# Kernel tuning notes

Measured on AMD Instinct MI355X. Metric: run time of the kernel, lower is better.

## Reference

```python
import jax, jax.numpy as jnp
import numpy as np

NUM_HEADS = 8
NUM_GROUPS = 32
EMB = 512
EPS = 1e-5


def setup_inputs() -> dict:
    key = jax.random.key(0)
    ks = jax.random.split(key, 12)
    B, C, H, W = 256, EMB, 16, 16
    s = 1.0 / np.sqrt(C)
    x = jax.random.normal(ks[0], (B, C, H, W), dtype=jnp.float32)
    Wq = jax.random.normal(ks[1], (C, EMB), dtype=jnp.float32) * s
    bq = jax.random.normal(ks[2], (EMB,), dtype=jnp.float32) * 0.01
    Wk = jax.random.normal(ks[3], (C, EMB), dtype=jnp.float32) * s
    bk = jax.random.normal(ks[4], (EMB,), dtype=jnp.float32) * 0.01
    Wv = jax.random.normal(ks[5], (C, EMB), dtype=jnp.float32) * s
    bv = jax.random.normal(ks[6], (EMB,), dtype=jnp.float32) * 0.01
    Wf = jax.random.normal(ks[7], (EMB, EMB), dtype=jnp.float32) * s
    bf = jax.random.normal(ks[8], (EMB,), dtype=jnp.float32) * 0.01
    gn_w = jnp.ones((EMB,), dtype=jnp.float32)
    gn_b = jnp.zeros((EMB,), dtype=jnp.float32)
    return {"x": x, "Wq": Wq, "bq": bq, "Wk": Wk, "bk": bk,
            "Wv": Wv, "bv": bv, "Wf": Wf, "bf": bf,
            "gn_w": gn_w, "gn_b": gn_b}


def reference(x, Wq, bq, Wk, bk, Wv, bv, Wf, bf, gn_w, gn_b):
    B, C, H, W = x.shape
    S = H * W
    nh = NUM_HEADS
    dh = EMB // nh
    xs = x.reshape(B, C, S).transpose(0, 2, 1)  # [B, S, C]
    q = (xs @ Wq + bq).reshape(B, S, nh, dh)
    k = (xs @ Wk + bk).reshape(B, S, nh, dh)
    v = (xs @ Wv + bv).reshape(B, S, nh, dh)
    scale = dh ** -0.5
    logits = jnp.einsum('bshd,bthd->bhst', q, k) * scale  # [B, nh, S, S]
    attn = jax.nn.softmax(logits, axis=-1)
    o = jnp.einsum('bhst,bthd->bshd', attn, v).reshape(B, S, EMB)
    o = o @ Wf + bf  # [B, S, EMB]
    y = o.transpose(0, 2, 1).reshape(B, EMB, H, W) + x  # residual
    # GroupNorm over (channels-within-group, H, W)
    G = NUM_GROUPS
    yg = y.reshape(B, G, EMB // G, H, W)
    mu = jnp.mean(yg, axis=(2, 3, 4), keepdims=True)
    var = jnp.var(yg, axis=(2, 3, 4), keepdims=True)
    yn = ((yg - mu) * jax.lax.rsqrt(var + EPS)).reshape(B, EMB, H, W)
    return yn * gn_w.reshape(1, EMB, 1, 1) + gn_b.reshape(1, EMB, 1, 1)
```

## Files before the change

### kernel.cpp

```cpp
#include <hip/hip_runtime.h>
#include <hip/hip_bf16.h>
#include <stdint.h>

#define B_  256
#define C_  512
#define S_  256
#define NH  8
#define DH  64

typedef float f32x4 __attribute__((ext_vector_type(4)));
typedef short s16x8 __attribute__((ext_vector_type(8)));

static __device__ __forceinline__ unsigned short f2bf(float f) {
  union { float f; unsigned u; } v; v.f = f;
  unsigned r = v.u + 0x7FFFu + ((v.u >> 16) & 1u);
  return (unsigned short)(r >> 16);
}

static __device__ __forceinline__ unsigned pk_bf16(float lo, float hi) {
  unsigned r;
  asm("v_cvt_pk_bf16_f32 %0, %1, %2" : "=v"(r) : "v"(lo), "v"(hi));
  return r;
}

static __device__ __forceinline__ void gload_lds16(const void* g, void* l) {
  __builtin_amdgcn_global_load_lds((const __attribute__((address_space(1))) void*)g,
                                   (__attribute__((address_space(3))) void*)l,
                                   16, 0, 0);
}

__global__ __launch_bounds__(256) void prep(const float* __restrict__ x,
                                            const float* __restrict__ Wq,
                                            const float* __restrict__ Wk,
                                            const float* __restrict__ Wv,
                                            const float* __restrict__ Wf,
                                            unsigned short* __restrict__ Whead,
                                            unsigned short* __restrict__ Wft,
                                            unsigned short* __restrict__ xs) {
  __shared__ float tile[64][65];
  int bid = blockIdx.x;
  int t = threadIdx.x;
  int tr = t >> 4;
  int tc = (t & 15) * 4;
  if (bid < 8192) {
    int b = bid >> 5, rem = bid & 31;
    int s0 = (rem & 3) * 64, c0 = (rem >> 2) * 64;
    const float* xb = x + (size_t)b * C_ * S_;
#pragma unroll
    for (int i = 0; i < 4; ++i) {
      int c = tr + i * 16;
      float4 v = *(const float4*)&xb[(size_t)(c0 + c) * S_ + s0 + tc];
      tile[c][tc + 0] = v.x; tile[c][tc + 1] = v.y;
      tile[c][tc + 2] = v.z; tile[c][tc + 3] = v.w;
    }
    __syncthreads();
    unsigned short* xsb = xs + (size_t)b * S_ * C_;
#pragma unroll
    for (int i = 0; i < 4; ++i) {
      int s = tr + i * 16;
      ushort4 o;
      o.x = f2bf(tile[tc + 0][s]); o.y = f2bf(tile[tc + 1][s]);
      o.z = f2bf(tile[tc + 2][s]); o.w = f2bf(tile[tc + 3][s]);
      *(ushort4*)&xsb[(size_t)(s0 + s) * C_ + c0 + tc] = o;
    }
  } else {
    int r = bid - 8192;
    int mat = r >> 6, r6 = r & 63;
    int n0 = (r6 & 7) * 64, c0 = (r6 >> 3) * 64;
    const float* src = (mat == 0) ? Wq : (mat == 1) ? Wk : (mat == 2) ? Wv : Wf;
#pragma unroll
    for (int i = 0; i < 4; ++i) {
      int c = tr + i * 16;
      float4 v = *(const float4*)&src[(size_t)(c0 + c) * 512 + n0 + tc];
      tile[c][tc + 0] = v.x; tile[c][tc + 1] = v.y;
      tile[c][tc + 2] = v.z; tile[c][tc + 3] = v.w;
    }
    __syncthreads();
    int h = n0 >> 6;
    unsigned short* dst = (mat < 3) ? (Whead + ((size_t)h * 192 + mat * 64) * 512)
                                    : (Wft + (size_t)n0 * 512);
#pragma unroll
    for (int i = 0; i < 4; ++i) {
      int nl = tr + i * 16;
      ushort4 o;
      o.x = f2bf(tile[tc + 0][nl]); o.y = f2bf(tile[tc + 1][nl]);
      o.z = f2bf(tile[tc + 2][nl]); o.w = f2bf(tile[tc + 3][nl]);
      *(ushort4*)&dst[(size_t)nl * 512 + c0 + tc] = o;
    }
  }
}

#define QKP 68
#define QOFF 0
#define KOFF 34816
#define VOFF 69632
__global__ __launch_bounds__(512) void qkvattn(const unsigned short* __restrict__ xs,
                                               const unsigned short* __restrict__ Whead,
                                               const float* __restrict__ bq,
                                               const float* __restrict__ bk,
                                               const float* __restrict__ bv,
                                               unsigned short* __restrict__ o) {
  __shared__ __align__(16) char lds[114688];
  int bid = blockIdx.x;
  int lin = (bid & 7) * 256 + (bid >> 3);
  int h = lin & 7, b = lin >> 3;
  int t = threadIdx.x, lane = t & 63, w = t >> 6;
  int l15 = lane & 15, l4 = lane >> 4;
  int wr = w >> 2, wc = w & 3;
  const unsigned short* xsb = xs + (size_t)b * S_ * C_;
  const unsigned short* wh  = Whead + (size_t)h * 192 * C_;

#define FSTAGE(kt, p)                                                         \
  {                                                                           \
    _Pragma("unroll")                                                         \
    for (int i = 0; i < 4; ++i) {                                             \
      int ch = i * 512 + t, r = ch >> 3, g = ch & 7;                          \
      int gs = g ^ (r & 7);                                                   \
      gload_lds16(xsb + (size_t)r * C_ + (kt) * 64 + gs * 8,                  \
                  lds + (p) * 57344 + ch * 16);                               \
    }                                                                         \
    _Pragma("unroll")                                                         \
    for (int i = 0; i < 3; ++i) {                                             \
      int ch = i * 512 + t, r = ch >> 3, g = ch & 7;                          \
      int gs = g ^ (r & 7);                                                   \
      gload_lds16(wh + (size_t)r * C_ + (kt) * 64 + gs * 8,                   \
                  lds + (p) * 57344 + 32768 + ch * 16);                       \
    }                                                                         \
  }

  f32x4 acc[8][3] = {};
  FSTAGE(0, 0);

  for (int kt = 0; kt < 8; ++kt) {
    if (kt < 7) FSTAGE(kt + 1, (kt + 1) & 1);
    if (kt < 7) asm volatile("s_waitcnt vmcnt(7)" ::: "memory");
    else        asm volatile("s_waitcnt vmcnt(0)" ::: "memory");
    __builtin_amdgcn_s_barrier();
    asm volatile("" ::: "memory");
    const char* Ab = lds + (kt & 1) * 57344;
    const char* Bb = Ab + 32768;
#pragma unroll
    for (int kk = 0; kk < 2; ++kk) {
      s16x8 afr[8], bfr[3];
#pragma unroll
      for (int fi = 0; fi < 8; ++fi) {
        int r = wr * 128 + fi * 16 + l15;
        afr[fi] = *(const s16x8*)(Ab + r * 128 + (((kk * 4 + l4) ^ (r & 7)) << 4));
      }
#pragma unroll
      for (int fj = 0; fj < 3; ++fj) {
        int r = wc * 48 + fj * 16 + l15;
        bfr[fj] = *(const s16x8*)(Bb + r * 128 + (((kk * 4 + l4) ^ (r & 7)) << 4));
      }
      __builtin_amdgcn_s_setprio(1);
#pragma unroll
      for (int fi = 0; fi < 8; ++fi)
#pragma unroll
        for (int fj = 0; fj < 3; ++fj)
          acc[fi][fj] = __builtin_amdgcn_mfma_f32_16x16x32_bf16(afr[fi], bfr[fj], acc[fi][fj], 0, 0, 0);
      __builtin_amdgcn_s_setprio(0);
    }
    __builtin_amdgcn_s_barrier();
  }
#undef FSTAGE

  unsigned short* Ql = (unsigned short*)(lds + QOFF);
  unsigned short* Kl = (unsigned short*)(lds + KOFF);
  unsigned short* Vl = (unsigned short*)(lds + VOFF);
  int h64 = h * 64;
#pragma unroll
  for (int fj = 0; fj < 3; ++fj) {
    int n = wc * 48 + fj * 16 + l15;
    int sel = n >> 6, d = n & 63;
    const float* bias = (sel == 0) ? bq : (sel == 1) ? bk : bv;
    float bias_v = bias[h64 + d];
    if (sel == 2) {
#pragma unroll
      for (int fi = 0; fi < 8; ++fi) {
        int s0 = wr * 128 + fi * 16 + l4 * 4;
        ushort4 o4;
        o4.x = f2bf(acc[fi][fj][0] + bias_v);
        o4.y = f2bf(acc[fi][fj][1] + bias_v);
        o4.z = f2bf(acc[fi][fj][2] + bias_v);
        o4.w = f2bf(acc[fi][fj][3] + bias_v);
        *(ushort4*)&Vl[d * 264 + s0] = o4;
      }
    } else {
      unsigned short* dstl = (sel == 0) ? Ql : Kl;
#pragma unroll
      for (int fi = 0; fi < 8; ++fi)
#pragma unroll
        for (int rg = 0; rg < 4; ++rg) {
          int s = wr * 128 + fi * 16 + l4 * 4 + rg;
          int row = s;
          if (sel == 1) {
            int s64 = s & 63, w32 = s64 & 31;
            row = (s & 192) + (s64 >> 5) * 32 + ((w32 >> 2) & 1) * 16 + (w32 >> 3) * 4 + (w32 & 3);
          }
          dstl[row * QKP + d] = f2bf(acc[fi][fj][rg] + bias_v);
        }
    }
  }
  __syncthreads();

  s16x8 qf[2][2];
#pragma unroll
  for (int fi = 0; fi < 2; ++fi)
#pragma unroll
    for (int kk = 0; kk < 2; ++kk) {
      int row = w * 32 + fi * 16 + l15;
      qf[fi][kk] = *(const s16x8*)((const char*)lds + QOFF + row * (QKP * 2) + kk * 64 + l4 * 16);
    }

  f32x4 acco[4][2] = {};
  float m_run[2] = {-3e38f, -3e38f}, l_run[2] = {0.f, 0.f};
  const float SCL = 0.125f * 1.44269504089f;

  for (int kb = 0; kb < 4; ++kb) {
    f32x4 accs[4][2] = {};
#pragma unroll
    for (int kk = 0; kk < 2; ++kk) {
      s16x8 kf[4];
#pragma unroll
      for (int fj = 0; fj < 4; ++fj)
        kf[fj] = *(const s16x8*)((const char*)lds + KOFF + (kb * 64 + fj * 16 + l15) * (QKP * 2) + kk * 64 + l4 * 16);
      __builtin_amdgcn_s_setprio(1);
#pragma unroll
      for (int fj = 0; fj < 4; ++fj)
#pragma unroll
        for (int fi = 0; fi < 2; ++fi)
          accs[fj][fi] = __builtin_amdgcn_mfma_f32_16x16x32_bf16(kf[fj], qf[fi][kk], accs[fj][fi], 0, 0, 0);
      __builtin_amdgcn_s_setprio(0);
    }
#pragma unroll
    for (int fi = 0; fi < 2; ++fi) {
      float m0[4];
#pragma unroll
      for (int fj = 0; fj < 4; ++fj)
        m0[fj] = fmaxf(fmaxf(accs[fj][fi][0], accs[fj][fi][1]),
                       fmaxf(accs[fj][fi][2], accs[fj][fi][3]));
      float mx = fmaxf(fmaxf(m0[0], m0[1]), fmaxf(m0[2], m0[3]));
      mx = fmaxf(mx, __shfl_xor(mx, 16, 64));
      mx = fmaxf(mx, __shfl_xor(mx, 32, 64));
      float mnew = fmaxf(m_run[fi], mx);
      float alpha = __builtin_amdgcn_exp2f((m_run[fi] - mnew) * SCL);
      m_run[fi] = mnew;
      float s0[4];
#pragma unroll
      for (int fj = 0; fj < 4; ++fj) {
#pragma unroll
        for (int rg = 0; rg < 4; ++rg) {
          float p = __builtin_amdgcn_exp2f((accs[fj][fi][rg] - mnew) * SCL);
          accs[fj][fi][rg] = p;
        }
        s0[fj] = (accs[fj][fi][0] + accs[fj][fi][1]) + (accs[fj][fi][2] + accs[fj][fi][3]);
      }
      float lsum = (s0[0] + s0[1]) + (s0[2] + s0[3]);
      lsum += __shfl_xor(lsum, 16, 64);
      lsum += __shfl_xor(lsum, 32, 64);
      l_run[fi] = l_run[fi] * alpha + lsum;
#pragma unroll
      for (int fd = 0; fd < 4; ++fd)
#pragma unroll
        for (int rg = 0; rg < 4; ++rg) acco[fd][fi][rg] *= alpha;
    }
#pragma unroll
    for (int kk2 = 0; kk2 < 2; ++kk2) {
      s16x8 vf[4];
#pragma unroll
      for (int fd = 0; fd < 4; ++fd)
        vf[fd] = *(const s16x8*)((const char*)lds + VOFF + (fd * 16 + l15) * 528 + kb * 128 + kk2 * 64 + l4 * 16);
#pragma unroll
      for (int fi = 0; fi < 2; ++fi) {
        union { unsigned u[4]; s16x8 v; } pb;
        pb.u[0] = pk_bf16(accs[2 * kk2][fi][0],     accs[2 * kk2][fi][1]);
        pb.u[1] = pk_bf16(accs[2 * kk2][fi][2],     accs[2 * kk2][fi][3]);
        pb.u[2] = pk_bf16(accs[2 * kk2 + 1][fi][0], accs[2 * kk2 + 1][fi][1]);
        pb.u[3] = pk_bf16(accs[2 * kk2 + 1][fi][2], accs[2 * kk2 + 1][fi][3]);
        __builtin_amdgcn_s_setprio(1);
#pragma unroll
        for (int fd = 0; fd < 4; ++fd)
          acco[fd][fi] = __builtin_amdgcn_mfma_f32_16x16x32_bf16(vf[fd], pb.v, acco[fd][fi], 0, 0, 0);
        __builtin_amdgcn_s_setprio(0);
      }
    }
  }

  unsigned short* ob = o + (size_t)b * S_ * C_ + h * DH;
#pragma unroll
  for (int fi = 0; fi < 2; ++fi) {
    float inv = 1.0f / l_run[fi];
    int qrow = w * 32 + fi * 16 + l15;
#pragma unroll
    for (int fd = 0; fd < 4; ++fd) {
      ushort4 s4;
      s4.x = f2bf(acco[fd][fi][0] * inv);
      s4.y = f2bf(acco[fd][fi][1] * inv);
      s4.z = f2bf(acco[fd][fi][2] * inv);
      s4.w = f2bf(acco[fd][fi][3] * inv);
      *(ushort4*)&ob[(size_t)qrow * C_ + fd * 16 + l4 * 4] = s4;
    }
  }
}

__global__ __launch_bounds__(512) void proj_gn(const unsigned short* __restrict__ o,
                                               const unsigned short* __restrict__ Wft,
                                               const float* __restrict__ bfp,
                                               const float* __restrict__ x,
                                               const float* __restrict__ gnw,
                                               const float* __restrict__ gnb,
                                               float* __restrict__ out) {
  __shared__ __align__(16) char plds[98304];
  __shared__ float red_s[128], red_q[128];
  __shared__ float mu_s[8], rs_s[8];
  int bid = blockIdx.x;
  int lin = (bid & 7) * 128 + (bid >> 3);
  int b = lin >> 2, ct = lin & 3;
  int t = threadIdx.x, lane = t & 63, w = t >> 6;
  int l15 = lane & 15, l4 = lane >> 4;
  int wc = w >> 2, wsq = w & 3;
  if (t < 128) { red_s[t] = 0.f; red_q[t] = 0.f; }
  f32x4 acc[4][4] = {};
  const unsigned short* wt = Wft + (size_t)ct * 128 * C_;
  const unsigned short* ob = o + (size_t)b * S_ * C_;

#define PSTAGE(kt, p)                                                         \
  {                                                                           \
    _Pragma("unroll")                                                         \
    for (int i = 0; i < 2; ++i) {                                             \
      int ch = i * 512 + t, r = ch >> 3, g = ch & 7;                          \
      int gs = g ^ (r & 7);                                                   \
      gload_lds16(wt + (size_t)r * C_ + (kt) * 64 + gs * 8,                   \
                  plds + (p) * 49152 + ch * 16);                              \
    }                                                                         \
    _Pragma("unroll")                                                         \
    for (int i = 0; i < 4; ++i) {                                             \
      int ch = i * 512 + t, r = ch >> 3, g = ch & 7;                          \
      int gs = g ^ (r & 7);                                                   \
      gload_lds16(ob + (size_t)r * C_ + (kt) * 64 + gs * 8,                   \
                  plds + (p) * 49152 + 16384 + ch * 16);                      \
    }                                                                         \
  }

  PSTAGE(0, 0);

  for (int kt = 0; kt < 8; ++kt) {
    if (kt < 7) PSTAGE(kt + 1, (kt + 1) & 1);
    if (kt < 7) asm volatile("s_waitcnt vmcnt(6)" ::: "memory");
    else        asm volatile("s_waitcnt vmcnt(0)" ::: "memory");
    __builtin_amdgcn_s_barrier();
    asm volatile("" ::: "memory");
    const char* Ab = plds + (kt & 1) * 49152;
    const char* Bb = Ab + 16384;
#pragma unroll
    for (int kk = 0; kk < 2; ++kk) {
      s16x8 af[4], bfr[4];
#pragma unroll
      for (int fi = 0; fi < 4; ++fi) {
        int r = wc * 64 + fi * 16 + l15;
        af[fi] = *(const s16x8*)(Ab + r * 128 + (((kk * 4 + l4) ^ (r & 7)) << 4));
      }
#pragma unroll
      for (int fj = 0; fj < 4; ++fj) {
        int r = wsq * 64 + fj * 16 + l15;
        bfr[fj] = *(const s16x8*)(Bb + r * 128 + (((kk * 4 + l4) ^ (r & 7)) << 4));
      }
      __builtin_amdgcn_s_setprio(1);
#pragma unroll
      for (int fi = 0; fi < 4; ++fi)
#pragma unroll
        for (int fj = 0; fj < 4; ++fj)
          acc[fi][fj] = __builtin_amdgcn_mfma_f32_16x16x32_bf16(af[fi], bfr[fj], acc[fi][fj], 0, 0, 0);
      __builtin_amdgcn_s_setprio(0);
    }
    __builtin_amdgcn_s_barrier();
  }
#undef PSTAGE

  const float* xb = x + (size_t)b * C_ * S_;
  int c_base = ct * 128 + wc * 64;
  int s_base = wsq * 64;
#pragma unroll
  for (int fi = 0; fi < 4; ++fi)
#pragma unroll
    for (int rg = 0; rg < 4; ++rg) {
      int c = c_base + fi * 16 + l4 * 4 + rg;
      float bias_v = bfp[c];
      float psum = 0.f, psq = 0.f;
#pragma unroll
      for (int fj = 0; fj < 4; ++fj) {
        int s = s_base + fj * 16 + l15;
        float y = acc[fi][fj][rg] + bias_v + xb[(size_t)c * S_ + s];
        acc[fi][fj][rg] = y;
        psum += y; psq += y * y;
      }
#pragma unroll
      for (int off = 1; off < 16; off <<= 1) {
        psum += __shfl_xor(psum, off, 64);
        psq += __shfl_xor(psq, off, 64);
      }
      if (l15 == 0) {
        int cl = c - ct * 128;
        atomicAdd(&red_s[cl], psum);
        atomicAdd(&red_q[cl], psq);
      }
    }
  __syncthreads();
  if (t < 8) {
    float s = 0.f, qq = 0.f;
#pragma unroll
    for (int i = 0; i < 16; ++i) { s += red_s[t * 16 + i]; qq += red_q[t * 16 + i]; }
    float mu = s * (1.0f / 4096.0f);
    float var = qq * (1.0f / 4096.0f) - mu * mu;
    mu_s[t] = mu;
    rs_s[t] = rsqrtf(var + 1e-5f);
  }
  __syncthreads();
  float* outb = out + (size_t)b * C_ * S_;
#pragma unroll
  for (int fi = 0; fi < 4; ++fi)
#pragma unroll
    for (int rg = 0; rg < 4; ++rg) {
      int c = c_base + fi * 16 + l4 * 4 + rg;
      int gl = (c - ct * 128) >> 4;
      float mu = mu_s[gl], rs = rs_s[gl];
      float gw = gnw[c], gb = gnb[c];
#pragma unroll
      for (int fj = 0; fj < 4; ++fj) {
        int s = s_base + fj * 16 + l15;
        outb[(size_t)c * S_ + s] = (acc[fi][fj][rg] - mu) * rs * gw + gb;
      }
    }
}

extern "C" void kernel_launch(void* const* d_in, const int* in_sizes, int n_in,
                              void* d_out, int out_size, void* d_ws, size_t ws_size,
                              hipStream_t stream) {
  const float* x   = (const float*)d_in[0];
  const float* Wq  = (const float*)d_in[1];
  const float* bq  = (const float*)d_in[2];
  const float* Wk  = (const float*)d_in[3];
  const float* bk  = (const float*)d_in[4];
  const float* Wv  = (const float*)d_in[5];
  const float* bv  = (const float*)d_in[6];
  const float* Wf  = (const float*)d_in[7];
  const float* bf  = (const float*)d_in[8];
  const float* gnw = (const float*)d_in[9];
  const float* gnb = (const float*)d_in[10];

  char* ws = (char*)d_ws;
  unsigned short* Whead = (unsigned short*)ws;
  unsigned short* Wft   = (unsigned short*)(ws + 0x180000);
  unsigned short* xs    = (unsigned short*)(ws + 0x200000);
  unsigned short* obuf  = (unsigned short*)(ws + 0x200000 + (size_t)B_ * S_ * C_ * 2);
  float* out = (float*)d_out;

  hipLaunchKernelGGL(prep, dim3(8448), dim3(256), 0, stream,
                     x, Wq, Wk, Wv, Wf, Whead, Wft, xs);
  hipLaunchKernelGGL(qkvattn, dim3(2048), dim3(512), 0, stream,
                     xs, Whead, bq, bk, bv, obuf);
  hipLaunchKernelGGL(proj_gn, dim3(1024), dim3(512), 0, stream,
                     obuf, Wft, bf, x, gnw, gnb, out);
}
```

Measured before the change: 315.3 us.

## Shrink proj_gn tiles to 64 channels and K-step 32 for higher occupancy

```diff
diff --git a/kernel.cpp b/kernel.cpp
--- a/kernel.cpp
+++ b/kernel.cpp
@@ -303,92 +303,92 @@
   }
 }
 
-__global__ __launch_bounds__(512) void proj_gn(const unsigned short* __restrict__ o,
-                                               const unsigned short* __restrict__ Wft,
-                                               const float* __restrict__ bfp,
-                                               const float* __restrict__ x,
-                                               const float* __restrict__ gnw,
-                                               const float* __restrict__ gnb,
-                                               float* __restrict__ out) {
-  __shared__ __align__(16) char plds[98304];
-  __shared__ float red_s[128], red_q[128];
-  __shared__ float mu_s[8], rs_s[8];
+__global__ __launch_bounds__(512, 4) void proj_gn(const unsigned short* __restrict__ o,
+                                                  const unsigned short* __restrict__ Wft,
+                                                  const float* __restrict__ bfp,
+                                                  const float* __restrict__ x,
+                                                  const float* __restrict__ gnw,
+                                                  const float* __restrict__ gnb,
+                                                  float* __restrict__ out) {
+  __shared__ __align__(16) char plds[40960];
+  __shared__ float red_s[64], red_q[64];
+  __shared__ float mu_s[4], rs_s[4];
   int bid = blockIdx.x;
-  int lin = (bid & 7) * 128 + (bid >> 3);
-  int b = lin >> 2, ct = lin & 3;
+  int lin = (bid & 7) * 256 + (bid >> 3);
+  int b = lin >> 3, ct = lin & 7;
   int t = threadIdx.x, lane = t & 63, w = t >> 6;
   int l15 = lane & 15, l4 = lane >> 4;
-  int wc = w >> 2, wsq = w & 3;
-  if (t < 128) { red_s[t] = 0.f; red_q[t] = 0.f; }
-  f32x4 acc[4][4] = {};
-  const unsigned short* wt = Wft + (size_t)ct * 128 * C_;
+  if (t < 64) { red_s[t] = 0.f; red_q[t] = 0.f; }
+  f32x4 acc[4][2] = {};
+  const unsigned short* wt = Wft + (size_t)ct * 64 * C_;
   const unsigned short* ob = o + (size_t)b * S_ * C_;
 
 #define PSTAGE(kt, p)                                                         \
   {                                                                           \
+    if (t < 256) {                                                            \
+      int r = t >> 2, g = t & 3;                                              \
+      int gs = g ^ ((r >> 1) & 3);                                            \
+      gload_lds16(wt + (size_t)r * C_ + (kt) * 32 + gs * 8,                   \
+                  plds + (p) * 20480 + t * 16);                               \
+    }                                                                         \
     _Pragma("unroll")                                                         \
     for (int i = 0; i < 2; ++i) {                                             \
-      int ch = i * 512 + t, r = ch >> 3, g = ch & 7;                          \
-      int gs = g ^ (r & 7);                                                   \
-      gload_lds16(wt + (size_t)r * C_ + (kt) * 64 + gs * 8,                   \
-                  plds + (p) * 49152 + ch * 16);                              \
+      int ch = i * 512 + t, r = ch >> 2, g = ch & 3;                          \
+      int gs = g ^ ((r >> 1) & 3);                                            \
+      gload_lds16(ob + (size_t)r * C_ + (kt) * 32 + gs * 8,                   \
+                  plds + (p) * 20480 + 4096 + ch * 16);                       \
     }                                                                         \
-    _Pragma("unroll")                                                         \
-    for (int i = 0; i < 4; ++i) {                                             \
-      int ch = i * 512 + t, r = ch >> 3, g = ch & 7;                          \
-      int gs = g ^ (r & 7);                                                   \
-      gload_lds16(ob + (size_t)r * C_ + (kt) * 64 + gs * 8,                   \
-                  plds + (p) * 49152 + 16384 + ch * 16);                      \
-    }                                                                         \
   }
 
   PSTAGE(0, 0);
 
-  for (int kt = 0; kt < 8; ++kt) {
-    if (kt < 7) PSTAGE(kt + 1, (kt + 1) & 1);
-    if (kt < 7) asm volatile("s_waitcnt vmcnt(6)" ::: "memory");
-    else        asm volatile("s_waitcnt vmcnt(0)" ::: "memory");
+  for (int kt = 0; kt < 16; ++kt) {
+    if (kt < 15) {
+      PSTAGE(kt + 1, (kt + 1) & 1);
+      if (t < 256) asm volatile("s_waitcnt vmcnt(3)" ::: "memory");
+      else         asm volatile("s_waitcnt vmcnt(2)" ::: "memory");
+    } else {
+      asm volatile("s_waitcnt vmcnt(0)" ::: "memory");
+    }
     __builtin_amdgcn_s_barrier();
     asm volatile("" ::: "memory");
-    const char* Ab = plds + (kt & 1) * 49152;
-    const char* Bb = Ab + 16384;
-#pragma unroll
-    for (int kk = 0; kk < 2; ++kk) {
-      s16x8 af[4], bfr[4];
-#pragma unroll
-      for (int fi = 0; fi < 4; ++fi) {
-        int r = wc * 64 + fi * 16 + l15;
-        af[fi] = *(const s16x8*)(Ab + r * 128 + (((kk * 4 + l4) ^ (r & 7)) << 4));
-      }
-#pragma unroll
-      for (int fj = 0; fj < 4; ++fj) {
-        int r = wsq * 64 + fj * 16 + l15;
-        bfr[fj] = *(const s16x8*)(Bb + r * 128 + (((kk * 4 + l4) ^ (r & 7)) << 4));
-      }
-      __builtin_amdgcn_s_setprio(1);
-#pragma unroll
-      for (int fi = 0; fi < 4; ++fi)
-#pragma unroll
-        for (int fj = 0; fj < 4; ++fj)
-          acc[fi][fj] = __builtin_amdgcn_mfma_f32_16x16x32_bf16(af[fi], bfr[fj], acc[fi][fj], 0, 0, 0);
-      __builtin_amdgcn_s_setprio(0);
-    }
+    const char* Ab = plds + (kt & 1) * 20480;
+    const char* Bb = Ab + 4096;
+    s16x8 af[4], bfr[2];
+#pragma unroll
+    for (int fi = 0; fi < 4; ++fi) {
+      int r = fi * 16 + l15;
+      af[fi] = *(const s16x8*)(Ab + r * 64 + ((l4 ^ ((r >> 1) & 3)) << 4));
+    }
+#pragma unroll
+    for (int fj = 0; fj < 2; ++fj) {
+      int r = w * 32 + fj * 16 + l15;
+      bfr[fj] = *(const s16x8*)(Bb + r * 64 + ((l4 ^ ((r >> 1) & 3)) << 4));
+    }
+    __builtin_amdgcn_s_setprio(1);
+#pragma unroll
+    for (int fi = 0; fi < 4; ++fi)
+#pragma unroll
+      for (int fj = 0; fj < 2; ++fj)
+        acc[fi][fj] = __builtin_amdgcn_mfma_f32_16x16x32_bf16(af[fi], bfr[fj], acc[fi][fj], 0, 0, 0);
+    __builtin_amdgcn_s_setprio(0);
     __builtin_amdgcn_s_barrier();
   }
 #undef PSTAGE
 
   const float* xb = x + (size_t)b * C_ * S_;
-  int c_base = ct * 128 + wc * 64;
-  int s_base = wsq * 64;
+  int c_base = ct * 64;
+  int s_base = w * 32;
 #pragma unroll
   for (int fi = 0; fi < 4; ++fi)
 #pragma unroll
     for (int rg = 0; rg < 4; ++rg) {
-      int c = c_base + fi * 16 + l4 * 4 + rg;
+      int cl = fi * 16 + l4 * 4 + rg;
+      int c = c_base + cl;
       float bias_v = bfp[c];
       float psum = 0.f, psq = 0.f;
 #pragma unroll
-      for (int fj = 0; fj < 4; ++fj) {
+      for (int fj = 0; fj < 2; ++fj) {
         int s = s_base + fj * 16 + l15;
         float y = acc[fi][fj][rg] + bias_v + xb[(size_t)c * S_ + s];
         acc[fi][fj][rg] = y;
@@ -400,13 +400,12 @@
         psq += __shfl_xor(psq, off, 64);
       }
       if (l15 == 0) {
-        int cl = c - ct * 128;
         atomicAdd(&red_s[cl], psum);
         atomicAdd(&red_q[cl], psq);
       }
     }
   __syncthreads();
-  if (t < 8) {
+  if (t < 4) {
     float s = 0.f, qq = 0.f;
 #pragma unroll
     for (int i = 0; i < 16; ++i) { s += red_s[t * 16 + i]; qq += red_q[t * 16 + i]; }
@@ -421,12 +420,13 @@
   for (int fi = 0; fi < 4; ++fi)
 #pragma unroll
     for (int rg = 0; rg < 4; ++rg) {
-      int c = c_base + fi * 16 + l4 * 4 + rg;
-      int gl = (c - ct * 128) >> 4;
+      int cl = fi * 16 + l4 * 4 + rg;
+      int c = c_base + cl;
+      int gl = cl >> 4;
       float mu = mu_s[gl], rs = rs_s[gl];
       float gw = gnw[c], gb = gnb[c];
 #pragma unroll
-      for (int fj = 0; fj < 4; ++fj) {
+      for (int fj = 0; fj < 2; ++fj) {
         int s = s_base + fj * 16 + l15;
         outb[(size_t)c * S_ + s] = (acc[fi][fj][rg] - mu) * rs * gw + gb;
       }
@@ -459,6 +459,6 @@
                      x, Wq, Wk, Wv, Wf, Whead, Wft, xs);
   hipLaunchKernelGGL(qkvattn, dim3(2048), dim3(512), 0, stream,
                      xs, Whead, bq, bk, bv, obuf);
-  hipLaunchKernelGGL(proj_gn, dim3(1024), dim3(512), 0, stream,
+  hipLaunchKernelGGL(proj_gn, dim3(2048), dim3(512), 0, stream,
                      obuf, Wft, bf, x, gnw, gnb, out);
 }
```

Result: no change. 314.7 us (-0.2%).
